# Optimization experiments

Hardware: AMD Instinct MI355X
Metric: run time of the kernel (lower is better)

The kernel has to match this reference:

```python
import jax, jax.numpy as jnp
import numpy as np

B, L, D = 16, 1024, 768

def setup_inputs() -> dict:
    key = jax.random.key(0)
    ks = jax.random.split(key, 6)
    s = 1.0 / np.sqrt(D)  # torch Linear default init scale
    return {
        "h": jax.random.normal(ks[0], (B, L, D), dtype=jnp.float32),
        "q": jax.random.normal(ks[1], (B, L, D), dtype=jnp.float32),
        "w1_w": jax.random.uniform(ks[2], (L, D), jnp.float32, -s, s),
        "w1_b": jax.random.uniform(ks[3], (L,), jnp.float32, -s, s),
        "w2_w": jax.random.uniform(ks[4], (L, D), jnp.float32, -s, s),
        "w2_b": jax.random.uniform(ks[5], (L,), jnp.float32, -s, s),
    }

def reference(h, q, w1_w, w1_b, w2_w, w2_b):
    # w1h: [B, L, l], w2q: [B, L, l] -> permuted [B, l, L]
    w1h = jnp.einsum('bsd,ld->bsl', h, w1_w) + w1_b
    w2q = jnp.einsum('btd,ld->btl', q, w2_w) + w2_b
    w3hq = jnp.einsum('bsd,btd->bst', h, q)           # [B, L, L]
    a = w1h + jnp.swapaxes(w2q, 1, 2) + w3hq          # [B, L, L]
    p = jax.nn.softmax(a, axis=2)
    c = jnp.einsum('bst,btd->bsd', p, q)              # [B, L, D]
    m = jnp.max(a, axis=2)                            # [B, L]
    p2 = jax.nn.softmax(m, axis=1)                    # [B, L]
    qc = h * p2[:, :, None]                           # [B, L, D]
    return jnp.concatenate([h, c, h * c, qc * c], axis=2)  # [B, L, 4D]
```

## Files before the change

kernel.cpp:

```cpp
#include <hip/hip_runtime.h>
#include <stdint.h>

#define B_  16
#define L_  1024
#define D_  768
#define K1_ 1536

typedef unsigned short u16;
typedef __attribute__((ext_vector_type(4))) float f32x4;
typedef __attribute__((ext_vector_type(8))) _Float16 f16x8;

__device__ __forceinline__ u16 f2h(float x){
    return __builtin_bit_cast(u16, (_Float16)x);
}
__device__ __forceinline__ float h2f(u16 x){
    return (float)__builtin_bit_cast(_Float16, x);
}

__device__ __forceinline__ void gload_lds16(const void* g, void* l){
    __builtin_amdgcn_global_load_lds((const __attribute__((address_space(1))) void*)g,
                                     (__attribute__((address_space(3))) void*)l, 16, 0, 0);
}

__global__ __launch_bounds__(256) void prep(const float* __restrict__ h, const float* __restrict__ q,
    const float* __restrict__ w1w, const float* __restrict__ w2w,
    u16* __restrict__ hH, u16* __restrict__ wH, u16* __restrict__ qH,
    u16* __restrict__ w1h, u16* __restrict__ qT, int b0, int nb)
{
    __shared__ float tile[32][33];
    int bb = blockIdx.z, bg = b0 + bb;
    int t0 = blockIdx.x * 32, d0 = blockIdx.y * 32;
    int tid = threadIdx.x;
    int r  = tid >> 3;
    int c4 = (tid & 7) * 4;
    int t = t0 + r, d = d0 + c4;
    size_t goff = (size_t)t * D_ + d;

    float4 qv  = *(const float4*)(q   + (size_t)bg * L_ * D_ + goff);
    float4 hv  = *(const float4*)(h   + (size_t)bg * L_ * D_ + goff);
    float4 w2v = *(const float4*)(w2w + goff);

    tile[r][c4 + 0] = qv.x; tile[r][c4 + 1] = qv.y;
    tile[r][c4 + 2] = qv.z; tile[r][c4 + 3] = qv.w;

    size_t o = ((size_t)bb * L_ + t) * D_ + d;
    ushort4 a;
    a.x = f2h(hv.x); a.y = f2h(hv.y); a.z = f2h(hv.z); a.w = f2h(hv.w);
    *(ushort4*)(hH + o) = a;
    a.x = f2h(hv.x + w2v.x); a.y = f2h(hv.y + w2v.y);
    a.z = f2h(hv.z + w2v.z); a.w = f2h(hv.w + w2v.w);
    *(ushort4*)(wH + o) = a;
    a.x = f2h(qv.x); a.y = f2h(qv.y); a.z = f2h(qv.z); a.w = f2h(qv.w);
    *(ushort4*)(qH + o) = a;
    if (bb == 0){
        float4 w1v = *(const float4*)(w1w + goff);
        a.x = f2h(w1v.x); a.y = f2h(w1v.y); a.z = f2h(w1v.z); a.w = f2h(w1v.w);
        *(ushort4*)(w1h + goff) = a;
    }
    __syncthreads();
    int dr = tid >> 3;
    int tc = (tid & 7) * 4;
    ushort4 b;
    b.x = f2h(tile[tc + 0][dr]); b.y = f2h(tile[tc + 1][dr]);
    b.z = f2h(tile[tc + 2][dr]); b.w = f2h(tile[tc + 3][dr]);
    *(ushort4*)(qT + (size_t)bb * D_ * L_ + (size_t)(d0 + dr) * L_ + t0 + tc) = b;
}

__global__ __launch_bounds__(256) void gemm1(
    const u16* __restrict__ hH, const u16* __restrict__ wH,
    const u16* __restrict__ qH, const u16* __restrict__ w1h,
    const float* __restrict__ w1b, const float* __restrict__ w2b,
    u16* __restrict__ aH, float* __restrict__ mT)
{
    __shared__ u16 ldsA[128 * 64];
    __shared__ u16 ldsB[128 * 64];
    int nwg = gridDim.x;
    int o = blockIdx.x;
    int wg = (o & 7) * (nwg >> 3) + (o >> 3);
    int bb = wg >> 6;
    int tl = wg & 63;
    int sm = tl >> 3, tn = tl & 7;
    int s0 = sm * 128, t0 = tn * 128;
    int tid = threadIdx.x;
    int lane = tid & 63, wid = tid >> 6;
    int wm = wid >> 1, wn = wid & 1;
    int l15 = lane & 15, l4 = lane >> 4;

    const u16* hHb = hH + (size_t)bb * L_ * D_;
    const u16* wHb = wH + (size_t)bb * L_ * D_;
    const u16* qHb = qH + (size_t)bb * L_ * D_;

    f32x4 acc[4][4];
    #pragma unroll
    for (int m = 0; m < 4; m++)
        #pragma unroll
        for (int n = 0; n < 4; n++)
            acc[m][n] = (f32x4){0.f, 0.f, 0.f, 0.f};

    for (int kb = 0; kb < K1_; kb += 64){
        bool inH = (kb < D_);
        const u16* Asrc = inH ? hHb : wHb;
        const u16* Bsrc = inH ? w1h : qHb;
        int koff = inH ? kb : (kb - D_);
        #pragma unroll
        for (int j = 0; j < 4; j++){
            int n = j * 256 + tid;
            int row = n >> 3, c = n & 7;
            int cc = c ^ (row & 7);
            int k = koff + cc * 8;
            gload_lds16(Asrc + (size_t)(s0 + row) * D_ + k, &ldsA[(j * 256 + wid * 64) * 8]);
            gload_lds16(Bsrc + (size_t)(t0 + row) * D_ + k, &ldsB[(j * 256 + wid * 64) * 8]);
        }
        __syncthreads();
        #pragma unroll
        for (int kk = 0; kk < 2; kk++){
            f16x8 af[4], bf[4];
            #pragma unroll
            for (int m = 0; m < 4; m++){
                int row = wm * 64 + m * 16 + l15;
                int c = kk * 4 + l4;
                af[m] = *(const f16x8*)&ldsA[(row * 8 + (c ^ (row & 7))) * 8];
            }
            #pragma unroll
            for (int n = 0; n < 4; n++){
                int row = wn * 64 + n * 16 + l15;
                int c = kk * 4 + l4;
                bf[n] = *(const f16x8*)&ldsB[(row * 8 + (c ^ (row & 7))) * 8];
            }
            #pragma unroll
            for (int m = 0; m < 4; m++)
                #pragma unroll
                for (int n = 0; n < 4; n++)
                    acc[m][n] = __builtin_amdgcn_mfma_f32_16x16x32_f16(af[m], bf[n], acc[m][n], 0, 0, 0);
        }
        __syncthreads();
    }

    u16* aRow = aH + (size_t)bb * L_ * L_;
    #pragma unroll
    for (int m = 0; m < 4; m++){
        #pragma unroll
        for (int r = 0; r < 4; r++){
            int s = s0 + wm * 64 + m * 16 + l4 * 4 + r;
            float w2v = w2b[s];
            float v[4];
            float tmax = -1e30f;
            #pragma unroll
            for (int n = 0; n < 4; n++){
                int tcol = t0 + wn * 64 + n * 16 + l15;
                v[n] = acc[m][n][r] + w1b[tcol] + w2v;
                tmax = fmaxf(tmax, v[n]);
            }
            #pragma unroll
            for (int o2 = 1; o2 < 16; o2 <<= 1)
                tmax = fmaxf(tmax, __shfl_xor(tmax, o2));
            #pragma unroll
            for (int n = 0; n < 4; n++){
                int tcol = t0 + wn * 64 + n * 16 + l15;
                aRow[(size_t)s * L_ + tcol] = f2h(v[n] - tmax);
            }
            if (l15 == 0)
                mT[((size_t)bb * L_ + s) * 16 + tn * 2 + wn] = tmax;
        }
    }
}

__global__ __launch_bounds__(1024) void p2k(const float* __restrict__ mT, float* __restrict__ mws,
                                            float* __restrict__ p2, int b0)
{
    __shared__ float red[16];
    int bb = blockIdx.x, bg = b0 + bb;
    int tid = threadIdx.x;
    const float4* rowv = (const float4*)(mT + ((size_t)bb * L_ + tid) * 16);
    float4 a0 = rowv[0], a1 = rowv[1], a2 = rowv[2], a3 = rowv[3];
    float v = fmaxf(fmaxf(fmaxf(a0.x, a0.y), fmaxf(a0.z, a0.w)),
             fmaxf(fmaxf(fmaxf(a1.x, a1.y), fmaxf(a1.z, a1.w)),
             fmaxf(fmaxf(fmaxf(a2.x, a2.y), fmaxf(a2.z, a2.w)),
                   fmaxf(fmaxf(a3.x, a3.y), fmaxf(a3.z, a3.w)))));
    mws[(size_t)bg * L_ + tid] = v;
    float mx = v;
    #pragma unroll
    for (int o = 32; o; o >>= 1) mx = fmaxf(mx, __shfl_xor(mx, o));
    if ((tid & 63) == 0) red[tid >> 6] = mx;
    __syncthreads();
    float m2 = red[0];
    #pragma unroll
    for (int i = 1; i < 16; i++) m2 = fmaxf(m2, red[i]);
    float e = __expf(v - m2);
    float sum = e;
    #pragma unroll
    for (int o = 32; o; o >>= 1) sum += __shfl_xor(sum, o);
    __syncthreads();
    if ((tid & 63) == 0) red[tid >> 6] = sum;
    __syncthreads();
    float st = 0.f;
    #pragma unroll
    for (int i = 0; i < 16; i++) st += red[i];
    p2[(size_t)bg * L_ + tid] = e / st;
}

__global__ __launch_bounds__(256) void rowsm(const u16* __restrict__ aH, u16* __restrict__ pB,
                                             const float* __restrict__ mws, const float* __restrict__ mT,
                                             int b0)
{
    __shared__ float red[4];
    int rowid = blockIdx.x;
    int bb = rowid >> 10, s = rowid & 1023;
    int tid = threadIdx.x;
    float mx = mws[(size_t)(b0 + bb) * L_ + s];
    float sub = mx - mT[(size_t)rowid * 16 + (tid >> 4)];
    const u16* row = aH + (size_t)rowid * L_;
    ushort4 pv = ((const ushort4*)row)[tid];
    float e0 = __expf(h2f(pv.x) - sub), e1 = __expf(h2f(pv.y) - sub);
    float e2 = __expf(h2f(pv.z) - sub), e3 = __expf(h2f(pv.w) - sub);
    float sum = e0 + e1 + e2 + e3;
    #pragma unroll
    for (int o = 32; o; o >>= 1) sum += __shfl_xor(sum, o);
    if ((tid & 63) == 0) red[tid >> 6] = sum;
    __syncthreads();
    sum = red[0] + red[1] + red[2] + red[3];
    float inv = 1.0f / sum;
    ushort4 pk;
    pk.x = f2h(e0 * inv); pk.y = f2h(e1 * inv); pk.z = f2h(e2 * inv); pk.w = f2h(e3 * inv);
    ((ushort4*)(pB + (size_t)rowid * L_))[tid] = pk;
}

__global__ __launch_bounds__(256) void gemm2(const u16* __restrict__ pB, const u16* __restrict__ qT,
    float* __restrict__ out, int b0)
{
    __shared__ u16 ldsA[128 * 64];
    __shared__ u16 ldsB[128 * 64];
    int nwg = gridDim.x;
    int o = blockIdx.x;
    int wg = (o & 7) * (nwg >> 3) + (o >> 3);
    int bb = wg / 48;
    int tl = wg % 48;
    int sm = tl / 6, dn = tl % 6;
    int s0 = sm * 128, d0 = dn * 128;
    int tid = threadIdx.x;
    int lane = tid & 63, wid = tid >> 6;
    int wm = wid >> 1, wn = wid & 1;
    int l15 = lane & 15, l4 = lane >> 4;

    const u16* Ab = pB + (size_t)bb * L_ * L_;
    const u16* Bb = qT + (size_t)bb * D_ * L_;

    f32x4 acc[4][4];
    #pragma unroll
    for (int m = 0; m < 4; m++)
        #pragma unroll
        for (int n = 0; n < 4; n++)
            acc[m][n] = (f32x4){0.f, 0.f, 0.f, 0.f};

    for (int kb = 0; kb < L_; kb += 64){
        #pragma unroll
        for (int j = 0; j < 4; j++){
            int n = j * 256 + tid;
            int row = n >> 3, c = n & 7;
            int cc = c ^ (row & 7);
            gload_lds16(Ab + (size_t)(s0 + row) * L_ + kb + cc * 8, &ldsA[(j * 256 + wid * 64) * 8]);
        }
        #pragma unroll
        for (int j = 0; j < 4; j++){
            int n = j * 256 + tid;
            int row = n >> 3, c = n & 7;
            int cc = c ^ (row & 7);
            gload_lds16(Bb + (size_t)(d0 + row) * L_ + kb + cc * 8, &ldsB[(j * 256 + wid * 64) * 8]);
        }
        __syncthreads();
        #pragma unroll
        for (int kk = 0; kk < 2; kk++){
            f16x8 af[4], bf[4];
            #pragma unroll
            for (int m = 0; m < 4; m++){
                int row = wm * 64 + m * 16 + l15;
                int c = kk * 4 + l4;
                af[m] = *(const f16x8*)&ldsA[(row * 8 + (c ^ (row & 7))) * 8];
            }
            #pragma unroll
            for (int n = 0; n < 4; n++){
                int row = wn * 64 + n * 16 + l15;
                int c = kk * 4 + l4;
                bf[n] = *(const f16x8*)&ldsB[(row * 8 + (c ^ (row & 7))) * 8];
            }
            #pragma unroll
            for (int m = 0; m < 4; m++)
                #pragma unroll
                for (int n = 0; n < 4; n++)
                    acc[m][n] = __builtin_amdgcn_mfma_f32_16x16x32_f16(af[m], bf[n], acc[m][n], 0, 0, 0);
        }
        __syncthreads();
    }

    float* oC = out + ((size_t)(b0 + bb) * L_) * (4 * D_) + D_;
    #pragma unroll
    for (int m = 0; m < 4; m++){
        int sbase = s0 + wm * 64 + m * 16 + l4 * 4;
        #pragma unroll
        for (int r = 0; r < 4; r++){
            int s = sbase + r;
            #pragma unroll
            for (int n = 0; n < 4; n++){
                int d = d0 + wn * 64 + n * 16 + l15;
                oC[(size_t)s * (4 * D_) + d] = acc[m][n][r];
            }
        }
    }
}

__global__ __launch_bounds__(192) void epi(const float* __restrict__ h,
    const float* __restrict__ p2, float* __restrict__ out, int b0)
{
    int rowid = blockIdx.x;
    int bb = rowid >> 10, s = rowid & 1023;
    int bg = b0 + bb;
    float p2v = p2[(size_t)bg * L_ + s];
    const float* hR = h + ((size_t)bg * L_ + s) * D_;
    float* oR = out + ((size_t)bg * L_ + s) * (4 * D_);
    int d = threadIdx.x * 4;
    float4 cv = *(const float4*)(oR + D_ + d);
    float4 hv = *(const float4*)(hR + d);
    float4 hc = {hv.x * cv.x, hv.y * cv.y, hv.z * cv.z, hv.w * cv.w};
    float4 qc = {p2v * hc.x, p2v * hc.y, p2v * hc.z, p2v * hc.w};
    *(float4*)(oR + d)          = hv;
    *(float4*)(oR + 2 * D_ + d) = hc;
    *(float4*)(oR + 3 * D_ + d) = qc;
}

extern "C" void kernel_launch(void* const* d_in, const int* in_sizes, int n_in,
                              void* d_out, int out_size, void* d_ws, size_t ws_size,
                              hipStream_t stream)
{
    const float* h   = (const float*)d_in[0];
    const float* q   = (const float*)d_in[1];
    const float* w1w = (const float*)d_in[2];
    const float* w1b = (const float*)d_in[3];
    const float* w2w = (const float*)d_in[4];
    const float* w2b = (const float*)d_in[5];
    float* out = (float*)d_out;

    const size_t szPlane = (size_t)L_ * D_ * 2;
    const size_t szM     = (size_t)B_ * L_ * 4;
    const size_t perB_aH = (size_t)L_ * L_ * 2;
    const size_t perB_pB = (size_t)L_ * L_ * 2;
    const size_t perB_mT = (size_t)L_ * 16 * 4;
    const size_t perB = 4 * szPlane + perB_aH + perB_pB + perB_mT;
    const size_t fixed = szPlane + 2 * szM;

    int NB = 1;
    if (ws_size > fixed){
        size_t nbc = (ws_size - fixed) / perB;
        NB = (nbc >= 16) ? 16 : (nbc < 1 ? 1 : (int)nbc);
    }

    char* p = (char*)d_ws;
    u16*   w1h  = (u16*)p;   p += szPlane;
    float* mws  = (float*)p; p += szM;
    float* p2   = (float*)p; p += szM;
    float* mT   = (float*)p; p += perB_mT * NB;
    u16*   hH   = (u16*)p;   p += szPlane * NB;
    u16*   wH   = (u16*)p;   p += szPlane * NB;
    u16*   qH   = (u16*)p;   p += szPlane * NB;
    u16*   qT   = (u16*)p;   p += szPlane * NB;
    u16*   pB   = (u16*)p;   p += perB_pB * NB;
    u16*   aH   = (u16*)p;

    for (int b0 = 0; b0 < B_; b0 += NB){
        int nb = (B_ - b0 < NB) ? (B_ - b0) : NB;
        prep  <<<dim3(32, 24, nb), 256, 0, stream>>>(h, q, w1w, w2w, hH, wH, qH, w1h, qT, b0, nb);
        gemm1 <<<dim3(64 * nb), 256, 0, stream>>>(hH, wH, qH, w1h, w1b, w2b, aH, mT);
        p2k   <<<dim3(nb), 1024, 0, stream>>>(mT, mws, p2, b0);
        rowsm <<<dim3(nb * 1024), 256, 0, stream>>>(aH, pB, mws, mT, b0);
        gemm2 <<<dim3(48 * nb), 256, 0, stream>>>(pB, qT, out, b0);
        epi   <<<dim3(nb * 1024), 192, 0, stream>>>(h, p2, out, b0);
    }
}
```

Before: 231.7 us.

## Fuse row softmax into GEMM epilogues with per-tile rescale factors

gemm1 now computes exp(v - tileMax) directly and stores per-64-column tile max and sum. p2k combines these into per-tile scale factors for each row. gemm2 applies the scales to a per-k-block partial accumulator, flash-style. This removes the separate rowsm kernel and one full L×L fp16 read/write pass. The cost is extra exps in gemm1, an extra accumulator set and FMAs per k-block in gemm2 with higher register pressure, and fp16 storage of unnormalized exps in [0,1].

```diff
diff --git a/kernel.cpp b/kernel.cpp
--- a/kernel.cpp
+++ b/kernel.cpp
@@ -70,7 +70,7 @@
     const u16* __restrict__ hH, const u16* __restrict__ wH,
     const u16* __restrict__ qH, const u16* __restrict__ w1h,
     const float* __restrict__ w1b, const float* __restrict__ w2b,
-    u16* __restrict__ aH, float* __restrict__ mT)
+    u16* __restrict__ pT, float* __restrict__ mT, float* __restrict__ sT)
 {
     __shared__ u16 ldsA[128 * 64];
     __shared__ u16 ldsB[128 * 64];
@@ -136,7 +136,7 @@
         __syncthreads();
     }
 
-    u16* aRow = aH + (size_t)bb * L_ * L_;
+    u16* pRow = pT + (size_t)bb * L_ * L_;
     #pragma unroll
     for (int m = 0; m < 4; m++){
         #pragma unroll
@@ -154,39 +154,53 @@
             #pragma unroll
             for (int o2 = 1; o2 < 16; o2 <<= 1)
                 tmax = fmaxf(tmax, __shfl_xor(tmax, o2));
+            float e[4];
+            float gsum = 0.f;
+            #pragma unroll
+            for (int n = 0; n < 4; n++){
+                e[n] = __expf(v[n] - tmax);
+                gsum += e[n];
+            }
             #pragma unroll
             for (int n = 0; n < 4; n++){
                 int tcol = t0 + wn * 64 + n * 16 + l15;
-                aRow[(size_t)s * L_ + tcol] = f2h(v[n] - tmax);
-            }
-            if (l15 == 0)
-                mT[((size_t)bb * L_ + s) * 16 + tn * 2 + wn] = tmax;
-        }
-    }
-}
-
-__global__ __launch_bounds__(1024) void p2k(const float* __restrict__ mT, float* __restrict__ mws,
-                                            float* __restrict__ p2, int b0)
+                pRow[(size_t)s * L_ + tcol] = f2h(e[n]);
+            }
+            #pragma unroll
+            for (int o2 = 1; o2 < 16; o2 <<= 1)
+                gsum += __shfl_xor(gsum, o2);
+            if (l15 == 0){
+                size_t mo = ((size_t)bb * L_ + s) * 16 + tn * 2 + wn;
+                mT[mo] = tmax;
+                sT[mo] = gsum;
+            }
+        }
+    }
+}
+
+__global__ __launch_bounds__(1024) void p2k(const float* __restrict__ mT, const float* __restrict__ sT,
+                                            float* __restrict__ p2, float* __restrict__ sc, int b0)
 {
     __shared__ float red[16];
     int bb = blockIdx.x, bg = b0 + bb;
     int tid = threadIdx.x;
-    const float4* rowv = (const float4*)(mT + ((size_t)bb * L_ + tid) * 16);
-    float4 a0 = rowv[0], a1 = rowv[1], a2 = rowv[2], a3 = rowv[3];
-    float v = fmaxf(fmaxf(fmaxf(a0.x, a0.y), fmaxf(a0.z, a0.w)),
-             fmaxf(fmaxf(fmaxf(a1.x, a1.y), fmaxf(a1.z, a1.w)),
-             fmaxf(fmaxf(fmaxf(a2.x, a2.y), fmaxf(a2.z, a2.w)),
-                   fmaxf(fmaxf(a3.x, a3.y), fmaxf(a3.z, a3.w)))));
-    mws[(size_t)bg * L_ + tid] = v;
+    const float4* mv = (const float4*)(mT + ((size_t)bb * L_ + tid) * 16);
+    float4 m0 = mv[0], m1 = mv[1], m2 = mv[2], m3 = mv[3];
+    float mj[16] = {m0.x, m0.y, m0.z, m0.w, m1.x, m1.y, m1.z, m1.w,
+                    m2.x, m2.y, m2.z, m2.w, m3.x, m3.y, m3.z, m3.w};
+    float v = mj[0];
+    #pragma unroll
+    for (int i = 1; i < 16; i++) v = fmaxf(v, mj[i]);
+
     float mx = v;
     #pragma unroll
     for (int o = 32; o; o >>= 1) mx = fmaxf(mx, __shfl_xor(mx, o));
     if ((tid & 63) == 0) red[tid >> 6] = mx;
     __syncthreads();
-    float m2 = red[0];
-    #pragma unroll
-    for (int i = 1; i < 16; i++) m2 = fmaxf(m2, red[i]);
-    float e = __expf(v - m2);
+    float m2g = red[0];
+    #pragma unroll
+    for (int i = 1; i < 16; i++) m2g = fmaxf(m2g, red[i]);
+    float e = __expf(v - m2g);
     float sum = e;
     #pragma unroll
     for (int o = 32; o; o >>= 1) sum += __shfl_xor(sum, o);
@@ -197,36 +211,27 @@
     #pragma unroll
     for (int i = 0; i < 16; i++) st += red[i];
     p2[(size_t)bg * L_ + tid] = e / st;
-}
-
-__global__ __launch_bounds__(256) void rowsm(const u16* __restrict__ aH, u16* __restrict__ pB,
-                                             const float* __restrict__ mws, const float* __restrict__ mT,
-                                             int b0)
-{
-    __shared__ float red[4];
-    int rowid = blockIdx.x;
-    int bb = rowid >> 10, s = rowid & 1023;
-    int tid = threadIdx.x;
-    float mx = mws[(size_t)(b0 + bb) * L_ + s];
-    float sub = mx - mT[(size_t)rowid * 16 + (tid >> 4)];
-    const u16* row = aH + (size_t)rowid * L_;
-    ushort4 pv = ((const ushort4*)row)[tid];
-    float e0 = __expf(h2f(pv.x) - sub), e1 = __expf(h2f(pv.y) - sub);
-    float e2 = __expf(h2f(pv.z) - sub), e3 = __expf(h2f(pv.w) - sub);
-    float sum = e0 + e1 + e2 + e3;
-    #pragma unroll
-    for (int o = 32; o; o >>= 1) sum += __shfl_xor(sum, o);
-    if ((tid & 63) == 0) red[tid >> 6] = sum;
-    __syncthreads();
-    sum = red[0] + red[1] + red[2] + red[3];
-    float inv = 1.0f / sum;
-    ushort4 pk;
-    pk.x = f2h(e0 * inv); pk.y = f2h(e1 * inv); pk.z = f2h(e2 * inv); pk.w = f2h(e3 * inv);
-    ((ushort4*)(pB + (size_t)rowid * L_))[tid] = pk;
-}
-
-__global__ __launch_bounds__(256) void gemm2(const u16* __restrict__ pB, const u16* __restrict__ qT,
-    float* __restrict__ out, int b0)
+
+    const float4* sv = (const float4*)(sT + ((size_t)bb * L_ + tid) * 16);
+    float4 s0v = sv[0], s1v = sv[1], s2v = sv[2], s3v = sv[3];
+    float sj[16] = {s0v.x, s0v.y, s0v.z, s0v.w, s1v.x, s1v.y, s1v.z, s1v.w,
+                    s2v.x, s2v.y, s2v.z, s2v.w, s3v.x, s3v.y, s3v.z, s3v.w};
+    float ej[16];
+    float S = 0.f;
+    #pragma unroll
+    for (int j = 0; j < 16; j++){
+        ej[j] = __expf(mj[j] - v);
+        S += sj[j] * ej[j];
+    }
+    float invS = 1.0f / S;
+    float* scb = sc + (size_t)bb * 16 * L_;
+    #pragma unroll
+    for (int j = 0; j < 16; j++)
+        scb[j * L_ + tid] = ej[j] * invS;
+}
+
+__global__ __launch_bounds__(256) void gemm2(const u16* __restrict__ pT, const u16* __restrict__ qT,
+    const float* __restrict__ sc, float* __restrict__ out, int b0)
 {
     __shared__ u16 ldsA[128 * 64];
     __shared__ u16 ldsB[128 * 64];
@@ -242,8 +247,9 @@
     int wm = wid >> 1, wn = wid & 1;
     int l15 = lane & 15, l4 = lane >> 4;
 
-    const u16* Ab = pB + (size_t)bb * L_ * L_;
+    const u16* Ab = pT + (size_t)bb * L_ * L_;
     const u16* Bb = qT + (size_t)bb * D_ * L_;
+    const float* scb = sc + (size_t)bb * 16 * L_;
 
     f32x4 acc[4][4];
     #pragma unroll
@@ -253,6 +259,7 @@
             acc[m][n] = (f32x4){0.f, 0.f, 0.f, 0.f};
 
     for (int kb = 0; kb < L_; kb += 64){
+        int jg = kb >> 6;
         #pragma unroll
         for (int j = 0; j < 4; j++){
             int n = j * 256 + tid;
@@ -267,7 +274,17 @@
             int cc = c ^ (row & 7);
             gload_lds16(Bb + (size_t)(d0 + row) * L_ + kb + cc * 8, &ldsB[(j * 256 + wid * 64) * 8]);
         }
+        f32x4 scv[4];
+        #pragma unroll
+        for (int m = 0; m < 4; m++)
+            scv[m] = *(const f32x4*)(scb + (size_t)jg * L_ + s0 + wm * 64 + m * 16 + l4 * 4);
         __syncthreads();
+        f32x4 acc2[4][4];
+        #pragma unroll
+        for (int m = 0; m < 4; m++)
+            #pragma unroll
+            for (int n = 0; n < 4; n++)
+                acc2[m][n] = (f32x4){0.f, 0.f, 0.f, 0.f};
         #pragma unroll
         for (int kk = 0; kk < 2; kk++){
             f16x8 af[4], bf[4];
@@ -287,8 +304,15 @@
             for (int m = 0; m < 4; m++)
                 #pragma unroll
                 for (int n = 0; n < 4; n++)
-                    acc[m][n] = __builtin_amdgcn_mfma_f32_16x16x32_f16(af[m], bf[n], acc[m][n], 0, 0, 0);
-        }
+                    acc2[m][n] = __builtin_amdgcn_mfma_f32_16x16x32_f16(af[m], bf[n], acc2[m][n], 0, 0, 0);
+        }
+        #pragma unroll
+        for (int m = 0; m < 4; m++)
+            #pragma unroll
+            for (int n = 0; n < 4; n++)
+                #pragma unroll
+                for (int r = 0; r < 4; r++)
+                    acc[m][n][r] += scv[m][r] * acc2[m][n][r];
         __syncthreads();
     }
 
@@ -341,11 +365,10 @@
 
     const size_t szPlane = (size_t)L_ * D_ * 2;
     const size_t szM     = (size_t)B_ * L_ * 4;
-    const size_t perB_aH = (size_t)L_ * L_ * 2;
-    const size_t perB_pB = (size_t)L_ * L_ * 2;
-    const size_t perB_mT = (size_t)L_ * 16 * 4;
-    const size_t perB = 4 * szPlane + perB_aH + perB_pB + perB_mT;
-    const size_t fixed = szPlane + 2 * szM;
+    const size_t perB_pT = (size_t)L_ * L_ * 2;
+    const size_t perB_s  = (size_t)L_ * 16 * 4;
+    const size_t perB = 4 * szPlane + perB_pT + 3 * perB_s;
+    const size_t fixed = szPlane + szM;
 
     int NB = 1;
     if (ws_size > fixed){
@@ -355,23 +378,22 @@
 
     char* p = (char*)d_ws;
     u16*   w1h  = (u16*)p;   p += szPlane;
-    float* mws  = (float*)p; p += szM;
     float* p2   = (float*)p; p += szM;
-    float* mT   = (float*)p; p += perB_mT * NB;
+    float* mT   = (float*)p; p += perB_s * NB;
+    float* sT   = (float*)p; p += perB_s * NB;
+    float* sc   = (float*)p; p += perB_s * NB;
     u16*   hH   = (u16*)p;   p += szPlane * NB;
     u16*   wH   = (u16*)p;   p += szPlane * NB;
     u16*   qH   = (u16*)p;   p += szPlane * NB;
     u16*   qT   = (u16*)p;   p += szPlane * NB;
-    u16*   pB   = (u16*)p;   p += perB_pB * NB;
-    u16*   aH   = (u16*)p;
+    u16*   pT   = (u16*)p;
 
     for (int b0 = 0; b0 < B_; b0 += NB){
         int nb = (B_ - b0 < NB) ? (B_ - b0) : NB;
         prep  <<<dim3(32, 24, nb), 256, 0, stream>>>(h, q, w1w, w2w, hH, wH, qH, w1h, qT, b0, nb);
-        gemm1 <<<dim3(64 * nb), 256, 0, stream>>>(hH, wH, qH, w1h, w1b, w2b, aH, mT);
-        p2k   <<<dim3(nb), 1024, 0, stream>>>(mT, mws, p2, b0);
-        rowsm <<<dim3(nb * 1024), 256, 0, stream>>>(aH, pB, mws, mT, b0);
-        gemm2 <<<dim3(48 * nb), 256, 0, stream>>>(pB, qT, out, b0);
+        gemm1 <<<dim3(64 * nb), 256, 0, stream>>>(hH, wH, qH, w1h, w1b, w2b, pT, mT, sT);
+        p2k   <<<dim3(nb), 1024, 0, stream>>>(mT, sT, p2, sc, b0);
+        gemm2 <<<dim3(48 * nb), 256, 0, stream>>>(pT, qT, sc, out, b0);
         epi   <<<dim3(nb * 1024), 192, 0, stream>>>(h, p2, out, b0);
     }
 }
```

Measured after the change: 236.9 us. 2.2% more time.
